# Kernel optimization log

Hardware: AMD Instinct MI355X
Metric: run time of the kernel (lower is better)

The kernel has to match this reference:

```python
import jax, jax.numpy as jnp
import numpy as np

N_NODES = 40000


def _gcn_conv(x, edge_index, W, b):
    """PyG GCNConv: add self-loops, symmetric degree normalization,
    linear transform, gather-scale-scatter aggregation, bias."""
    n = x.shape[0]
    loops = jnp.arange(n, dtype=edge_index.dtype)
    src = jnp.concatenate([edge_index[0], loops])  # [E+N]
    dst = jnp.concatenate([edge_index[1], loops])  # [E+N]
    ones = jnp.ones(src.shape[0], dtype=x.dtype)
    deg = jax.ops.segment_sum(ones, dst, num_segments=n)  # in-degree incl. self-loop
    dinv = jnp.where(deg > 0, jax.lax.rsqrt(deg), 0.0)
    norm = dinv[src] * dinv[dst]  # [E+N]
    h = x @ W  # [n, out]
    msg = h[src] * norm[:, None]  # [E+N, out] gather + scale
    out = jax.ops.segment_sum(msg, dst, num_segments=n)  # scatter-add
    return out + b


def setup_inputs() -> dict:
    key = jax.random.key(0)
    k = jax.random.split(key, 6)
    n, din, dh, dout = N_NODES, 128, 128, 64
    x = jax.random.normal(k[0], (n, din), dtype=jnp.float32)
    edge_index = jax.random.randint(k[1], (2, 640000), 0, n, dtype=jnp.int64)
    W1 = jax.random.normal(k[2], (din, dh), dtype=jnp.float32) / np.sqrt(din)
    b1 = jnp.zeros((dh,), dtype=jnp.float32)
    W2 = jax.random.normal(k[3], (dh, dout), dtype=jnp.float32) / np.sqrt(dh)
    b2 = jnp.zeros((dout,), dtype=jnp.float32)
    return {"x": x, "edge_index": edge_index, "W1": W1, "b1": b1, "W2": W2, "b2": b2}


def reference(x, edge_index, W1, b1, W2, b2):
    h = jax.nn.relu(_gcn_conv(x, edge_index, W1, b1))
    return _gcn_conv(h, edge_index, W2, b2)
```

## Files before the change

### kernel.cpp

```cpp
#include <hip/hip_runtime.h>
#include <hip/hip_fp16.h>


#define N_NODES 40000
#define DIN 128
#define DH 128
#define DOUT 64
#define NEDGES 640000
#define CAP 64
#define NBUCKET 2560
#define I4_PER_CHUNK 500
#define NODES_PER_XCD 5000
#define NCVT 1250
#define NWT 8

typedef _Float16 f16x8 __attribute__((ext_vector_type(8)));
typedef float f32x4 __attribute__((ext_vector_type(4)));

__global__ __launch_bounds__(256) void k_bkt_cvt(
    const float* __restrict__ x, _Float16* __restrict__ xh,
    const int4* __restrict__ src4, const int4* __restrict__ dst4,
    int* __restrict__ deg, unsigned short* __restrict__ ssrc,
    const float* __restrict__ W1, const float* __restrict__ W2,
    _Float16* __restrict__ WT1, _Float16* __restrict__ WT2)
{
    if (blockIdx.x < NBUCKET) {
        const int xg = blockIdx.x & 7;
        const int c  = blockIdx.x >> 3;
        const int lo = xg * NODES_PER_XCD, hi = lo + NODES_PER_XCD;
        const int e0 = c * I4_PER_CHUNK, e1 = e0 + I4_PER_CHUNK;
        for (int e = e0 + threadIdx.x; e < e1; e += 256) {
            int4 d = dst4[e];
            int4 s = src4[e];
            if (d.x >= lo && d.x < hi) {
                int p = atomicAdd(&deg[d.x], 1);
                if (p < CAP) ssrc[d.x * CAP + p] = (unsigned short)s.x;
            }
            if (d.y >= lo && d.y < hi) {
                int p = atomicAdd(&deg[d.y], 1);
                if (p < CAP) ssrc[d.y * CAP + p] = (unsigned short)s.y;
            }
            if (d.z >= lo && d.z < hi) {
                int p = atomicAdd(&deg[d.z], 1);
                if (p < CAP) ssrc[d.z * CAP + p] = (unsigned short)s.z;
            }
            if (d.w >= lo && d.w < hi) {
                int p = atomicAdd(&deg[d.w], 1);
                if (p < CAP) ssrc[d.w * CAP + p] = (unsigned short)s.w;
            }
        }
    } else if (blockIdx.x < NBUCKET + NCVT) {
        const size_t base = ((size_t)(blockIdx.x - NBUCKET) * 256 + threadIdx.x) * 16;
        float4 a0 = *(const float4*)(x + base);
        float4 a1 = *(const float4*)(x + base + 4);
        float4 a2 = *(const float4*)(x + base + 8);
        float4 a3 = *(const float4*)(x + base + 12);
        f16x8 o0 = { (_Float16)a0.x, (_Float16)a0.y, (_Float16)a0.z, (_Float16)a0.w,
                     (_Float16)a1.x, (_Float16)a1.y, (_Float16)a1.z, (_Float16)a1.w };
        f16x8 o1 = { (_Float16)a2.x, (_Float16)a2.y, (_Float16)a2.z, (_Float16)a2.w,
                     (_Float16)a3.x, (_Float16)a3.y, (_Float16)a3.z, (_Float16)a3.w };
        *(f16x8*)(xh + base)     = o0;
        *(f16x8*)(xh + base + 8) = o1;
    } else {
        const int b = blockIdx.x - NBUCKET - NCVT;
        for (int i = b * 256 + threadIdx.x; i < DIN * DH; i += NWT * 256) {
            int k = i >> 7, nn = i & 127;
            WT1[nn * DIN + k] = (_Float16)W1[i];
        }
        for (int i = b * 256 + threadIdx.x; i < DH * DOUT; i += NWT * 256) {
            int k = i >> 6, nn = i & 63;
            WT2[nn * DH + k] = (_Float16)W2[i];
        }
    }
}

__global__ __launch_bounds__(256) void k_agg_g12(
    const int* __restrict__ deg, const unsigned short* __restrict__ ssrc,
    const _Float16* __restrict__ xh, const float* __restrict__ b1,
    const _Float16* __restrict__ WT1, const _Float16* __restrict__ WT2,
    _Float16* __restrict__ h2)
{
    __shared__ _Float16 ys[16][136];
    __shared__ _Float16 zs[16][136];
    const int w = threadIdx.x >> 6;
    const int lane = threadIdx.x & 63;
    const int g  = lane >> 4;
    const int gl = lane & 15;
    const int node0 = blockIdx.x * 16;
    const int node = node0 + w * 4 + g;

    const int dg = deg[node];
    const int cnt = min(dg, CAP);
    const float dn = rsqrtf((float)(dg + 1));

    float ac[8];
    {
        f16x8 self = *(const f16x8*)(xh + (size_t)node * DIN + gl * 8);
#pragma unroll
        for (int j = 0; j < 8; ++j) ac[j] = dn * (float)self[j];
    }
    int mc = cnt;
    mc = max(mc, __shfl_xor(mc, 16));
    mc = max(mc, __shfl_xor(mc, 32));

    const unsigned short* bin = ssrc + (size_t)node * CAP;
    for (int e = 0; e < mc; e += 4) {
        unsigned long long pk = *(const unsigned long long*)(bin + e);
        int s0 = (int)(pk & 0xFFFF),         s1 = (int)((pk >> 16) & 0xFFFF);
        int s2 = (int)((pk >> 32) & 0xFFFF), s3 = (int)((pk >> 48) & 0xFFFF);
        s0 = (e + 0 < cnt) ? s0 : 0;
        s1 = (e + 1 < cnt) ? s1 : 0;
        s2 = (e + 2 < cnt) ? s2 : 0;
        s3 = (e + 3 < cnt) ? s3 : 0;
        f16x8 r0 = *(const f16x8*)(xh + (size_t)s0 * DIN + gl * 8);
        f16x8 r1 = *(const f16x8*)(xh + (size_t)s1 * DIN + gl * 8);
        f16x8 r2 = *(const f16x8*)(xh + (size_t)s2 * DIN + gl * 8);
        f16x8 r3 = *(const f16x8*)(xh + (size_t)s3 * DIN + gl * 8);
        float w0 = (e + 0 < cnt) ? rsqrtf((float)(deg[s0] + 1)) : 0.f;
        float w1 = (e + 1 < cnt) ? rsqrtf((float)(deg[s1] + 1)) : 0.f;
        float w2 = (e + 2 < cnt) ? rsqrtf((float)(deg[s2] + 1)) : 0.f;
        float w3 = (e + 3 < cnt) ? rsqrtf((float)(deg[s3] + 1)) : 0.f;
#pragma unroll
        for (int j = 0; j < 8; ++j)
            ac[j] += (w0 * (float)r0[j] + w1 * (float)r1[j])
                   + (w2 * (float)r2[j] + w3 * (float)r3[j]);
    }
    {
        f16x8 o;
#pragma unroll
        for (int j = 0; j < 8; ++j) o[j] = (_Float16)(dn * ac[j]);
        *(f16x8*)&ys[w * 4 + g][gl * 8] = o;
    }
    __syncthreads();

    const int m = lane & 15, quad = lane >> 4;
#pragma unroll
    for (int t = 0; t < 2; ++t) {
        const int nt = w * 2 + t;
        f32x4 acc1 = (f32x4){0.f, 0.f, 0.f, 0.f};
#pragma unroll
        for (int ks = 0; ks < 4; ++ks) {
            f16x8 a = *(const f16x8*)&ys[m][ks * 32 + quad * 8];
            f16x8 b = *(const f16x8*)(WT1 + (size_t)(nt * 16 + m) * DIN + ks * 32 + quad * 8);
            acc1 = __builtin_amdgcn_mfma_f32_16x16x32_f16(a, b, acc1, 0, 0, 0);
        }
        float bias = b1[nt * 16 + m];
#pragma unroll
        for (int r = 0; r < 4; ++r) {
            float v = acc1[r] + bias;
            zs[quad * 4 + r][nt * 16 + m] = (_Float16)(v > 0.f ? v : 0.f);
        }
    }
    __syncthreads();

    {
        f32x4 acc2 = (f32x4){0.f, 0.f, 0.f, 0.f};
#pragma unroll
        for (int ks = 0; ks < 4; ++ks) {
            f16x8 a = *(const f16x8*)&zs[m][ks * 32 + quad * 8];
            f16x8 b = *(const f16x8*)(WT2 + (size_t)(w * 16 + m) * DH + ks * 32 + quad * 8);
            acc2 = __builtin_amdgcn_mfma_f32_16x16x32_f16(a, b, acc2, 0, 0, 0);
        }
#pragma unroll
        for (int r = 0; r < 4; ++r) {
            int nrow = node0 + quad * 4 + r;
            float dnr = rsqrtf((float)(deg[nrow] + 1));
            h2[(size_t)nrow * DOUT + w * 16 + m] = (_Float16)(acc2[r] * dnr);
        }
    }
}

__global__ __launch_bounds__(256) void k_agg2(
    const int* __restrict__ deg, const unsigned short* __restrict__ ssrc,
    const _Float16* __restrict__ h2, const float* __restrict__ b2,
    float* __restrict__ out)
{
    const int w = threadIdx.x >> 6;
    const int lane = threadIdx.x & 63;
    const int g  = lane >> 3;
    const int gl = lane & 7;
    const int node = blockIdx.x * 32 + w * 8 + g;

    const int dg = deg[node];
    const int cnt = min(dg, CAP);
    const float dn = rsqrtf((float)(dg + 1));

    float ac[8];
    {
        f16x8 self = *(const f16x8*)(h2 + (size_t)node * DOUT + gl * 8);
#pragma unroll
        for (int j = 0; j < 8; ++j) ac[j] = (float)self[j];
    }
    int mc = cnt;
    mc = max(mc, __shfl_xor(mc, 8));
    mc = max(mc, __shfl_xor(mc, 16));
    mc = max(mc, __shfl_xor(mc, 32));

    const unsigned short* bin = ssrc + (size_t)node * CAP;
    for (int e = 0; e < mc; e += 4) {
        unsigned long long pk = *(const unsigned long long*)(bin + e);
        int s0 = (int)(pk & 0xFFFF),         s1 = (int)((pk >> 16) & 0xFFFF);
        int s2 = (int)((pk >> 32) & 0xFFFF), s3 = (int)((pk >> 48) & 0xFFFF);
        s0 = (e + 0 < cnt) ? s0 : 0;
        s1 = (e + 1 < cnt) ? s1 : 0;
        s2 = (e + 2 < cnt) ? s2 : 0;
        s3 = (e + 3 < cnt) ? s3 : 0;
        float m0 = (e + 0 < cnt) ? 1.f : 0.f;
        float m1 = (e + 1 < cnt) ? 1.f : 0.f;
        float m2 = (e + 2 < cnt) ? 1.f : 0.f;
        float m3 = (e + 3 < cnt) ? 1.f : 0.f;
        f16x8 r0 = *(const f16x8*)(h2 + (size_t)s0 * DOUT + gl * 8);
        f16x8 r1 = *(const f16x8*)(h2 + (size_t)s1 * DOUT + gl * 8);
        f16x8 r2 = *(const f16x8*)(h2 + (size_t)s2 * DOUT + gl * 8);
        f16x8 r3 = *(const f16x8*)(h2 + (size_t)s3 * DOUT + gl * 8);
#pragma unroll
        for (int j = 0; j < 8; ++j)
            ac[j] += (m0 * (float)r0[j] + m1 * (float)r1[j])
                   + (m2 * (float)r2[j] + m3 * (float)r3[j]);
    }
    float4 ba = *(const float4*)(b2 + gl * 8);
    float4 bb = *(const float4*)(b2 + gl * 8 + 4);
    float4 o0 = { dn * ac[0] + ba.x, dn * ac[1] + ba.y,
                  dn * ac[2] + ba.z, dn * ac[3] + ba.w };
    float4 o1 = { dn * ac[4] + bb.x, dn * ac[5] + bb.y,
                  dn * ac[6] + bb.z, dn * ac[7] + bb.w };
    float* orow = out + (size_t)node * DOUT + gl * 8;
    *(float4*)orow = o0;
    *(float4*)(orow + 4) = o1;
}

extern "C" void kernel_launch(void* const* d_in, const int* in_sizes, int n_in,
                              void* d_out, int out_size, void* d_ws, size_t ws_size,
                              hipStream_t stream) {
    const float* x  = (const float*)d_in[0];
    const int*   ei = (const int*)d_in[1];
    const float* W1 = (const float*)d_in[2];
    const float* b1 = (const float*)d_in[3];
    const float* W2 = (const float*)d_in[4];
    const float* b2 = (const float*)d_in[5];
    float* out = (float*)d_out;

    const int n = N_NODES, E = NEDGES;
    const int* src = ei;
    const int* dst = ei + E;

    char* ws = (char*)d_ws;
    int*            deg  = (int*)(ws + 0);
    _Float16*       WT1  = (_Float16*)(ws + 163840);
    _Float16*       WT2  = (_Float16*)(ws + 196608);
    unsigned short* ssrc = (unsigned short*)(ws + 212992);
    _Float16*       xh   = (_Float16*)(ws + 5332992);
    _Float16*       h2   = (_Float16*)(ws + 15572992);

    hipMemsetAsync(deg, 0, N_NODES * sizeof(int), stream);
    k_bkt_cvt <<<NBUCKET + NCVT + NWT, 256, 0, stream>>>(x, xh, (const int4*)src,
                                                         (const int4*)dst, deg, ssrc,
                                                         W1, W2, WT1, WT2);
    k_agg_g12 <<<n / 16, 256, 0, stream>>>(deg, ssrc, xh, b1, WT1, WT2, h2);
    k_agg2    <<<n / 32, 256, 0, stream>>>(deg, ssrc, h2, b2, out);
}
```

Before: 166.7 us.

## Prescale fp16 features by source degree norm and unroll gathers to eight edges

Adds a separate pass that multiplies each fp16 input row by its own rsqrt(deg+1). This removes the per-edge deg lookup and rsqrt from the first aggregation loop, which now uses only a 0/1 mask. Both aggregation loops also load eight packed source indices per iteration instead of four, and point padded slots at the node itself instead of row 0, to expose more memory-level parallelism. The trade-off is an extra kernel launch plus one read and write of the whole fp16 feature buffer, more registers per thread, and one extra fp16 rounding of the scaled features.

After: 158.8 us. 4.7% less time.

```diff
diff --git a/kernel.cpp b/kernel.cpp
--- a/kernel.cpp
+++ b/kernel.cpp
@@ -74,6 +74,19 @@
     }
 }
 
+__global__ __launch_bounds__(256) void k_scale(
+    _Float16* __restrict__ xh, const int* __restrict__ deg)
+{
+    int idx = blockIdx.x * 256 + threadIdx.x;
+    int row = idx >> 4;
+    float dn = rsqrtf((float)(deg[row] + 1));
+    f16x8 v = *(f16x8*)(xh + (size_t)idx * 8);
+    f16x8 o;
+#pragma unroll
+    for (int j = 0; j < 8; ++j) o[j] = (_Float16)((float)v[j] * dn);
+    *(f16x8*)(xh + (size_t)idx * 8) = o;
+}
+
 __global__ __launch_bounds__(256) void k_agg_g12(
     const int* __restrict__ deg, const unsigned short* __restrict__ ssrc,
     const _Float16* __restrict__ xh, const float* __restrict__ b1,
@@ -97,33 +110,42 @@
     {
         f16x8 self = *(const f16x8*)(xh + (size_t)node * DIN + gl * 8);
 #pragma unroll
-        for (int j = 0; j < 8; ++j) ac[j] = dn * (float)self[j];
+        for (int j = 0; j < 8; ++j) ac[j] = (float)self[j];
     }
     int mc = cnt;
     mc = max(mc, __shfl_xor(mc, 16));
     mc = max(mc, __shfl_xor(mc, 32));
 
     const unsigned short* bin = ssrc + (size_t)node * CAP;
-    for (int e = 0; e < mc; e += 4) {
-        unsigned long long pk = *(const unsigned long long*)(bin + e);
-        int s0 = (int)(pk & 0xFFFF),         s1 = (int)((pk >> 16) & 0xFFFF);
-        int s2 = (int)((pk >> 32) & 0xFFFF), s3 = (int)((pk >> 48) & 0xFFFF);
-        s0 = (e + 0 < cnt) ? s0 : 0;
-        s1 = (e + 1 < cnt) ? s1 : 0;
-        s2 = (e + 2 < cnt) ? s2 : 0;
-        s3 = (e + 3 < cnt) ? s3 : 0;
+    for (int e = 0; e < mc; e += 8) {
+        uint4 pk = *(const uint4*)(bin + e);
+        int s0 = (int)(pk.x & 0xFFFF), s1 = (int)(pk.x >> 16);
+        int s2 = (int)(pk.y & 0xFFFF), s3 = (int)(pk.y >> 16);
+        int s4 = (int)(pk.z & 0xFFFF), s5 = (int)(pk.z >> 16);
+        int s6 = (int)(pk.w & 0xFFFF), s7 = (int)(pk.w >> 16);
+        float m0 = (e + 0 < cnt) ? 1.f : 0.f;  s0 = (e + 0 < cnt) ? s0 : node;
+        float m1 = (e + 1 < cnt) ? 1.f : 0.f;  s1 = (e + 1 < cnt) ? s1 : node;
+        float m2 = (e + 2 < cnt) ? 1.f : 0.f;  s2 = (e + 2 < cnt) ? s2 : node;
+        float m3 = (e + 3 < cnt) ? 1.f : 0.f;  s3 = (e + 3 < cnt) ? s3 : node;
+        float m4 = (e + 4 < cnt) ? 1.f : 0.f;  s4 = (e + 4 < cnt) ? s4 : node;
+        float m5 = (e + 5 < cnt) ? 1.f : 0.f;  s5 = (e + 5 < cnt) ? s5 : node;
+        float m6 = (e + 6 < cnt) ? 1.f : 0.f;  s6 = (e + 6 < cnt) ? s6 : node;
+        float m7 = (e + 7 < cnt) ? 1.f : 0.f;  s7 = (e + 7 < cnt) ? s7 : node;
         f16x8 r0 = *(const f16x8*)(xh + (size_t)s0 * DIN + gl * 8);
         f16x8 r1 = *(const f16x8*)(xh + (size_t)s1 * DIN + gl * 8);
         f16x8 r2 = *(const f16x8*)(xh + (size_t)s2 * DIN + gl * 8);
         f16x8 r3 = *(const f16x8*)(xh + (size_t)s3 * DIN + gl * 8);
-        float w0 = (e + 0 < cnt) ? rsqrtf((float)(deg[s0] + 1)) : 0.f;
-        float w1 = (e + 1 < cnt) ? rsqrtf((float)(deg[s1] + 1)) : 0.f;
-        float w2 = (e + 2 < cnt) ? rsqrtf((float)(deg[s2] + 1)) : 0.f;
-        float w3 = (e + 3 < cnt) ? rsqrtf((float)(deg[s3] + 1)) : 0.f;
-#pragma unroll
-        for (int j = 0; j < 8; ++j)
-            ac[j] += (w0 * (float)r0[j] + w1 * (float)r1[j])
-                   + (w2 * (float)r2[j] + w3 * (float)r3[j]);
+        f16x8 r4 = *(const f16x8*)(xh + (size_t)s4 * DIN + gl * 8);
+        f16x8 r5 = *(const f16x8*)(xh + (size_t)s5 * DIN + gl * 8);
+        f16x8 r6 = *(const f16x8*)(xh + (size_t)s6 * DIN + gl * 8);
+        f16x8 r7 = *(const f16x8*)(xh + (size_t)s7 * DIN + gl * 8);
+#pragma unroll
+        for (int j = 0; j < 8; ++j) {
+            ac[j] += (m0 * (float)r0[j] + m1 * (float)r1[j])
+                   + (m2 * (float)r2[j] + m3 * (float)r3[j]);
+            ac[j] += (m4 * (float)r4[j] + m5 * (float)r5[j])
+                   + (m6 * (float)r6[j] + m7 * (float)r7[j]);
+        }
     }
     {
         f16x8 o;
@@ -197,26 +219,35 @@
     mc = max(mc, __shfl_xor(mc, 32));
 
     const unsigned short* bin = ssrc + (size_t)node * CAP;
-    for (int e = 0; e < mc; e += 4) {
-        unsigned long long pk = *(const unsigned long long*)(bin + e);
-        int s0 = (int)(pk & 0xFFFF),         s1 = (int)((pk >> 16) & 0xFFFF);
-        int s2 = (int)((pk >> 32) & 0xFFFF), s3 = (int)((pk >> 48) & 0xFFFF);
-        s0 = (e + 0 < cnt) ? s0 : 0;
-        s1 = (e + 1 < cnt) ? s1 : 0;
-        s2 = (e + 2 < cnt) ? s2 : 0;
-        s3 = (e + 3 < cnt) ? s3 : 0;
-        float m0 = (e + 0 < cnt) ? 1.f : 0.f;
-        float m1 = (e + 1 < cnt) ? 1.f : 0.f;
-        float m2 = (e + 2 < cnt) ? 1.f : 0.f;
-        float m3 = (e + 3 < cnt) ? 1.f : 0.f;
+    for (int e = 0; e < mc; e += 8) {
+        uint4 pk = *(const uint4*)(bin + e);
+        int s0 = (int)(pk.x & 0xFFFF), s1 = (int)(pk.x >> 16);
+        int s2 = (int)(pk.y & 0xFFFF), s3 = (int)(pk.y >> 16);
+        int s4 = (int)(pk.z & 0xFFFF), s5 = (int)(pk.z >> 16);
+        int s6 = (int)(pk.w & 0xFFFF), s7 = (int)(pk.w >> 16);
+        float m0 = (e + 0 < cnt) ? 1.f : 0.f;  s0 = (e + 0 < cnt) ? s0 : node;
+        float m1 = (e + 1 < cnt) ? 1.f : 0.f;  s1 = (e + 1 < cnt) ? s1 : node;
+        float m2 = (e + 2 < cnt) ? 1.f : 0.f;  s2 = (e + 2 < cnt) ? s2 : node;
+        float m3 = (e + 3 < cnt) ? 1.f : 0.f;  s3 = (e + 3 < cnt) ? s3 : node;
+        float m4 = (e + 4 < cnt) ? 1.f : 0.f;  s4 = (e + 4 < cnt) ? s4 : node;
+        float m5 = (e + 5 < cnt) ? 1.f : 0.f;  s5 = (e + 5 < cnt) ? s5 : node;
+        float m6 = (e + 6 < cnt) ? 1.f : 0.f;  s6 = (e + 6 < cnt) ? s6 : node;
+        float m7 = (e + 7 < cnt) ? 1.f : 0.f;  s7 = (e + 7 < cnt) ? s7 : node;
         f16x8 r0 = *(const f16x8*)(h2 + (size_t)s0 * DOUT + gl * 8);
         f16x8 r1 = *(const f16x8*)(h2 + (size_t)s1 * DOUT + gl * 8);
         f16x8 r2 = *(const f16x8*)(h2 + (size_t)s2 * DOUT + gl * 8);
         f16x8 r3 = *(const f16x8*)(h2 + (size_t)s3 * DOUT + gl * 8);
-#pragma unroll
-        for (int j = 0; j < 8; ++j)
+        f16x8 r4 = *(const f16x8*)(h2 + (size_t)s4 * DOUT + gl * 8);
+        f16x8 r5 = *(const f16x8*)(h2 + (size_t)s5 * DOUT + gl * 8);
+        f16x8 r6 = *(const f16x8*)(h2 + (size_t)s6 * DOUT + gl * 8);
+        f16x8 r7 = *(const f16x8*)(h2 + (size_t)s7 * DOUT + gl * 8);
+#pragma unroll
+        for (int j = 0; j < 8; ++j) {
             ac[j] += (m0 * (float)r0[j] + m1 * (float)r1[j])
                    + (m2 * (float)r2[j] + m3 * (float)r3[j]);
+            ac[j] += (m4 * (float)r4[j] + m5 * (float)r5[j])
+                   + (m6 * (float)r6[j] + m7 * (float)r7[j]);
+        }
     }
     float4 ba = *(const float4*)(b2 + gl * 8);
     float4 bb = *(const float4*)(b2 + gl * 8 + 4);
@@ -256,6 +287,7 @@
     k_bkt_cvt <<<NBUCKET + NCVT + NWT, 256, 0, stream>>>(x, xh, (const int4*)src,
                                                          (const int4*)dst, deg, ssrc,
                                                          W1, W2, WT1, WT2);
+    k_scale   <<<(N_NODES * DIN / 8) / 256, 256, 0, stream>>>(xh, deg);
     k_agg_g12 <<<n / 16, 256, 0, stream>>>(deg, ssrc, xh, b1, WT1, WT2, h2);
     k_agg2    <<<n / 32, 256, 0, stream>>>(deg, ssrc, h2, b2, out);
 }
```
